# Kernel tuning notes

Hardware: AMD Instinct MI355X
Metric: run time of the kernel (lower is better)

## Reference

```python
import jax, jax.numpy as jnp
import numpy as np

NUM = 5   # grid intervals
K = 3     # spline order


def make_grid(in_dim, num=NUM, k=K, lo=-1.0, hi=1.0):
    # pykan: linspace over [lo,hi] with num+1 knots, extended by k on each side
    g = np.linspace(lo, hi, num + 1)
    h = (g[-1] - g[0]) / num
    left = g[0] - h * np.arange(k, 0, -1)
    right = g[-1] + h * np.arange(1, k + 1)
    g = np.concatenate([left, g, right])  # (num + 2k + 1,)
    return jnp.asarray(np.broadcast_to(g, (in_dim, g.shape[0])), dtype=jnp.float32)


def b_batch(x, grid, k=K):
    # x: (B, in), grid: (in, G) -> B-spline bases (B, in, G-k-1) via Cox-de Boor
    xe = x[:, :, None]                      # (B, in, 1)
    g = grid[None]                          # (1, in, G)
    B = ((xe >= g[:, :, :-1]) & (xe < g[:, :, 1:])).astype(x.dtype)
    for ki in range(1, k + 1):
        B = ((xe - g[:, :, :-(ki + 1)]) / (g[:, :, ki:-1] - g[:, :, :-(ki + 1)]) * B[:, :, :-1]
             + (g[:, :, ki + 1:] - xe) / (g[:, :, ki + 1:] - g[:, :, 1:-ki]) * B[:, :, 1:])
    return jnp.nan_to_num(B)


def kan_layer(x, grid, coef, scale_base, scale_sp, mask, k=K):
    # x: (B, in); coef: (in, out, num+k); scales/mask: (in, out)
    base = jax.nn.silu(x)                             # (B, in)
    Bsp = b_batch(x, grid, k)                         # (B, in, num+k)
    y = jnp.einsum('bik,iok->bio', Bsp, coef)         # spline curves (B, in, out)
    y = scale_base[None] * base[:, :, None] + scale_sp[None] * y
    y = mask[None] * y
    return jnp.sum(y, axis=1)                         # (B, out)


def setup_inputs() -> dict:
    key = jax.random.key(0)
    ks = jax.random.split(key, 10)
    B, IN, HID, OUT = 4096, 1024, 256, 128
    KC = NUM + K  # coef count per edge
    x = jax.random.normal(ks[0], (B, IN), dtype=jnp.float32)
    W1 = jax.random.normal(ks[1], (HID, IN), dtype=jnp.float32) / np.sqrt(IN)
    b1 = jnp.zeros((HID,), dtype=jnp.float32)
    grid1 = make_grid(HID)
    coef1 = jax.random.normal(ks[2], (HID, HID, KC), dtype=jnp.float32) * 0.1
    sb1 = jax.random.normal(ks[3], (HID, HID), dtype=jnp.float32) / np.sqrt(HID)
    sp1 = jnp.ones((HID, HID), dtype=jnp.float32) / np.sqrt(HID)
    mask1 = jnp.ones((HID, HID), dtype=jnp.float32)
    grid2 = make_grid(HID)
    coef2 = jax.random.normal(ks[4], (HID, OUT, KC), dtype=jnp.float32) * 0.1
    sb2 = jax.random.normal(ks[5], (HID, OUT), dtype=jnp.float32) / np.sqrt(HID)
    sp2 = jnp.ones((HID, OUT), dtype=jnp.float32) / np.sqrt(HID)
    mask2 = jnp.ones((HID, OUT), dtype=jnp.float32)
    return {"x": x, "W1": W1, "b1": b1,
            "grid1": grid1, "coef1": coef1, "sb1": sb1, "sp1": sp1, "mask1": mask1,
            "grid2": grid2, "coef2": coef2, "sb2": sb2, "sp2": sp2, "mask2": mask2}


def reference(x, W1, b1, grid1, coef1, sb1, sp1, mask1, grid2, coef2, sb2, sp2, mask2):
    h = x @ W1.T + b1                                  # fc1
    h = kan_layer(h, grid1, coef1, sb1, sp1, mask1)    # kanl1
    out = kan_layer(h, grid2, coef2, sb2, sp2, mask2)  # kanl2
    return out
```

## Files before the change

### kernel.cpp

```cpp
#include <hip/hip_runtime.h>
#include <math.h>

typedef unsigned short u16;
typedef u16 u16x4 __attribute__((ext_vector_type(4)));
typedef u16 u16x8 __attribute__((ext_vector_type(8)));
typedef float f32x4 __attribute__((ext_vector_type(4)));
typedef float f32x16 __attribute__((ext_vector_type(16)));
typedef __bf16 bf16x8 __attribute__((ext_vector_type(8)));

#define KC 8
#define K2L 2304

__device__ __forceinline__ u16 f2bf_rne(float f) {
  unsigned u = __float_as_uint(f);
  u += 0x7FFFu + ((u >> 16) & 1u);
  return (u16)(u >> 16);
}
__device__ __forceinline__ float bf2f(u16 h) {
  return __uint_as_float(((unsigned)h) << 16);
}

__device__ __forceinline__ void gload16(const u16* g, u16* l) {
  __builtin_amdgcn_global_load_lds(
      (const __attribute__((address_space(1))) unsigned*)g,
      (__attribute__((address_space(3))) unsigned*)l, 16, 0, 0);
}

template <int N>
__device__ __forceinline__ void vmwait() {
  if constexpr (N == 0)      asm volatile("s_waitcnt vmcnt(0)" ::: "memory");
  else if constexpr (N == 4) asm volatile("s_waitcnt vmcnt(4)" ::: "memory");
  else if constexpr (N == 8) asm volatile("s_waitcnt vmcnt(8)" ::: "memory");
  else static_assert(N == 0, "unsupported vmcnt literal");
}

__device__ __forceinline__ void split4(const float* X, u16* hi, u16* lo, int i) {
  f32x4 v = ((const f32x4*)X)[i];
  u16x4 h, l;
#pragma unroll
  for (int c = 0; c < 4; ++c) {
    u16 hb = f2bf_rne(v[c]);
    h[c] = hb;
    l[c] = f2bf_rne(v[c] - bf2f(hb));
  }
  ((u16x4*)hi)[i] = h;
  ((u16x4*)lo)[i] = l;
}
__device__ __forceinline__ void wc_one(const float* coef, const float* sb, const float* sp,
                                       const float* mask, u16* W, int N, int idx) {
  int o = idx / K2L;
  int r = idx - o * K2L;
  int i = r / 9;
  int c = r - i * 9;
  int io = i * N + o;
  float m = mask[io];
  float v = (c == 0) ? m * sb[io] : m * sp[io] * coef[(size_t)io * KC + (c - 1)];
  W[idx] = f2bf_rne(v);
}

__global__ void prep_kernel(const float* __restrict__ x, const float* __restrict__ W1,
                            const float* __restrict__ coef1, const float* __restrict__ sb1,
                            const float* __restrict__ sp1, const float* __restrict__ mask1,
                            const float* __restrict__ coef2, const float* __restrict__ sb2,
                            const float* __restrict__ sp2, const float* __restrict__ mask2,
                            u16* __restrict__ xs_hi, u16* __restrict__ xs_lo,
                            u16* __restrict__ w1_hi, u16* __restrict__ w1_lo,
                            u16* __restrict__ wc1, u16* __restrict__ wc2) {
  const int b = blockIdx.x, tid = threadIdx.x;
  if (b < 4096) {
    split4(x, xs_hi, xs_lo, b * 256 + tid);
  } else if (b < 4096 + 256) {
    split4(W1, w1_hi, w1_lo, (b - 4096) * 256 + tid);
  } else if (b < 4096 + 256 + 2304) {
    wc_one(coef1, sb1, sp1, mask1, wc1, 256, (b - 4352) * 256 + tid);
  } else {
    wc_one(coef2, sb2, sp2, mask2, wc2, 128, (b - 6656) * 256 + tid);
  }
}

struct Spl {
  float g[12];
  float d1[11], d2[10], d3[9];
};
__device__ __forceinline__ void spl_init(const float* __restrict__ grid, Spl& sp) {
#pragma unroll
  for (int j = 0; j < 12; ++j) sp.g[j] = grid[j];
#pragma unroll
  for (int j = 0; j < 11; ++j) sp.d1[j] = 1.0f / (sp.g[j + 1] - sp.g[j]);
#pragma unroll
  for (int j = 0; j < 10; ++j) sp.d2[j] = 1.0f / (sp.g[j + 2] - sp.g[j]);
#pragma unroll
  for (int j = 0; j < 9; ++j) sp.d3[j] = 1.0f / (sp.g[j + 3] - sp.g[j]);
}
__device__ __forceinline__ void expand_one(float v, const Spl& sp, u16* dst) {
  float Bv[11];
#pragma unroll
  for (int j = 0; j < 11; ++j) Bv[j] = (v >= sp.g[j] && v < sp.g[j + 1]) ? 1.0f : 0.0f;
#pragma unroll
  for (int j = 0; j < 10; ++j)
    Bv[j] = (v - sp.g[j]) * sp.d1[j] * Bv[j] + (sp.g[j + 2] - v) * sp.d1[j + 1] * Bv[j + 1];
#pragma unroll
  for (int j = 0; j < 9; ++j)
    Bv[j] = (v - sp.g[j]) * sp.d2[j] * Bv[j] + (sp.g[j + 3] - v) * sp.d2[j + 1] * Bv[j + 1];
#pragma unroll
  for (int j = 0; j < 8; ++j)
    Bv[j] = (v - sp.g[j]) * sp.d3[j] * Bv[j] + (sp.g[j + 4] - v) * sp.d3[j + 1] * Bv[j + 1];
  dst[0] = f2bf_rne(v / (1.0f + __expf(-v)));
#pragma unroll
  for (int k = 0; k < 8; ++k) dst[1 + k] = f2bf_rne(Bv[k]);
}

template <int NREG, bool EXPAND>
__global__ __launch_bounds__(512) void gemm8w(
    const u16* __restrict__ A0, const u16* __restrict__ A1,
    const u16* __restrict__ B0, const u16* __restrict__ B1,
    const float* __restrict__ bias, const float* __restrict__ grid,
    void* __restrict__ outv, int M, int N, int K, int nsteps) {
  constexpr int ASZ = 64 * 128;
  constexpr int BUF_U16 = 2 * ASZ;
  __shared__ __align__(16) u16 smu[4 * BUF_U16];

  const int tid = threadIdx.x;
  const int lane = tid & 63;
  const int wid = tid >> 6;
  const int q = wid & 3;
  const int kg = wid >> 2;

  const int nb = N >> 6;
  const int nwg = (M >> 6) * nb;
  const int bid = blockIdx.x;
  const int swz = (bid & 7) * (nwg >> 3) + (bid >> 3);
  const int tm = (swz / nb) << 6;
  const int tn = (swz % nb) << 6;

  const u16* pA0 = A0 + (size_t)tm * K;
  const u16* pB0 = B0 + (size_t)tn * K;
  const u16* pA1 = (NREG == 3) ? A1 + (size_t)tm * K : nullptr;
  const u16* pB1 = (NREG == 3) ? B1 + (size_t)tn * K : nullptr;

  auto srcOff = [&](int c) -> int {
    int r = c >> 4, sl = c & 15;
    return r * K + (((sl ^ (r & 15)) & 15) << 3);
  };
  const int s0 = srcOff(tid);
  const int s1 = srcOff(tid + 512);

  const int wm = (q >> 1) * 32;
  const int wn = (q & 1) * 32;
  const int lr = lane & 31;
  const int khf = lane >> 5;

  int offA[4], offB[4];
#pragma unroll
  for (int s = 0; s < 4; ++s) {
    int slice = kg * 4 + s;
    int rowA = wm + lr;
    int rowB = wn + lr;
    offA[s] = rowA * 128 + ((((slice * 2 + khf) ^ (rowA & 15)) & 15) << 3);
    offB[s] = rowB * 128 + ((((slice * 2 + khf) ^ (rowB & 15)) & 15) << 3);
  }

  auto stage = [&](int buf, int step) {
    int kk;
    const u16 *Ab, *Bb;
    if constexpr (NREG == 3) {
      int reg = step >> 3;
      kk = (step & 7) << 7;
      Ab = (reg == 2) ? pA1 : pA0;
      Bb = (reg == 1) ? pB1 : pB0;
    } else {
      kk = step << 7;
      Ab = pA0;
      Bb = pB0;
    }
    u16* sb = smu + buf * BUF_U16;
    gload16(Ab + s0 + kk, sb + wid * 512);
    gload16(Ab + s1 + kk, sb + 4096 + wid * 512);
    gload16(Bb + s0 + kk, sb + ASZ + wid * 512);
    gload16(Bb + s1 + kk, sb + ASZ + 4096 + wid * 512);
  };

  f32x16 acc0 = {}, acc1 = {};
  stage(0, 0);
  stage(1, 1);
  for (int i = 0; i < nsteps; ++i) {
    if (i + 2 < nsteps) {
      stage((i + 2) & 3, i + 2);
      vmwait<8>();
    } else if (i + 1 < nsteps) {
      vmwait<4>();
    } else {
      vmwait<0>();
    }
    __builtin_amdgcn_sched_barrier(0);
    __builtin_amdgcn_s_barrier();
    __builtin_amdgcn_sched_barrier(0);

    const u16* sb = smu + (i & 3) * BUF_U16;
    bf16x8 af[4], bfr[4];
#pragma unroll
    for (int s = 0; s < 4; ++s) {
      af[s] = *(const bf16x8*)(sb + offA[s]);
      bfr[s] = *(const bf16x8*)(sb + ASZ + offB[s]);
    }
#pragma unroll
    for (int s = 0; s < 4; ++s) {
      f32x16& ac = (s & 1) ? acc1 : acc0;
      ac = __builtin_amdgcn_mfma_f32_32x32x16_bf16(af[s], bfr[s], ac, 0, 0, 0);
    }
  }
  f32x16 accv = acc0 + acc1;

  const int rbase = 4 * khf;

  float* Fr = (float*)smu;
  __syncthreads();
  if (kg == 1) {
#pragma unroll
    for (int r = 0; r < 16; ++r) {
      int row = wm + rbase + (r & 3) + 8 * (r >> 2);
      Fr[row * 64 + wn + lr] = accv[r];
    }
  }
  __syncthreads();
  if (kg == 0) {
#pragma unroll
    for (int r = 0; r < 16; ++r) {
      int row = wm + rbase + (r & 3) + 8 * (r >> 2);
      accv[r] += Fr[row * 64 + wn + lr];
    }
  }

  if constexpr (EXPAND) {
    Spl sp;
    spl_init(grid, sp);
    __syncthreads();
    u16* Fl = smu;
    if (kg == 0) {
      int col = wn + lr;
      float bv = bias ? bias[tn + col] : 0.0f;
#pragma unroll
      for (int r = 0; r < 16; ++r) {
        int row = wm + rbase + (r & 3) + 8 * (r >> 2);
        expand_one(accv[r] + bv, sp, Fl + (size_t)row * (64 * 9) + col * 9);
      }
    }
    __syncthreads();
    u16* Fout = (u16*)outv;
    const size_t fstride = (size_t)N * 9;
#pragma unroll
    for (int ch = tid; ch < 4608; ch += 512) {
      int r = ch / 72, o = ch - r * 72;
      *(u16x8*)(Fout + (size_t)(tm + r) * fstride + (size_t)tn * 9 + o * 8) =
          *(const u16x8*)(Fl + (size_t)ch * 8);
    }
  } else {
    if (kg == 0) {
      float* Cp = (float*)outv;
      const int cbase = tn + wn + lr;
#pragma unroll
      for (int r = 0; r < 16; ++r) {
        int row = tm + wm + rbase + (r & 3) + 8 * (r >> 2);
        Cp[(size_t)row * N + cbase] = accv[r];
      }
    }
  }
}

extern "C" void kernel_launch(void* const* d_in, const int* in_sizes, int n_in,
                              void* d_out, int out_size, void* d_ws, size_t ws_size,
                              hipStream_t stream) {
  (void)in_sizes; (void)n_in; (void)out_size; (void)ws_size;
  const float* x     = (const float*)d_in[0];
  const float* W1    = (const float*)d_in[1];
  const float* b1    = (const float*)d_in[2];
  const float* grid1 = (const float*)d_in[3];
  const float* coef1 = (const float*)d_in[4];
  const float* sb1   = (const float*)d_in[5];
  const float* sp1   = (const float*)d_in[6];
  const float* mask1 = (const float*)d_in[7];
  const float* grid2 = (const float*)d_in[8];
  const float* coef2 = (const float*)d_in[9];
  const float* sb2   = (const float*)d_in[10];
  const float* sp2   = (const float*)d_in[11];
  const float* mask2 = (const float*)d_in[12];
  float* outp = (float*)d_out;

  char* ws = (char*)d_ws;
  size_t off = 0;
  auto alloc = [&](size_t bytes) {
    char* p = ws + off;
    off += (bytes + 255) & ~(size_t)255;
    return (void*)p;
  };
  u16* xs_hi  = (u16*)alloc((size_t)4096 * 1024 * 2);
  u16* xs_lo  = (u16*)alloc((size_t)4096 * 1024 * 2);
  u16* w1_hi  = (u16*)alloc((size_t)256 * 1024 * 2);
  u16* w1_lo  = (u16*)alloc((size_t)256 * 1024 * 2);
  u16* wc1    = (u16*)alloc((size_t)256 * K2L * 2);
  u16* wc2    = (u16*)alloc((size_t)128 * K2L * 2);
  u16* F1     = (u16*)alloc((size_t)4096 * K2L * 2);
  u16* F2     = (u16*)alloc((size_t)4096 * K2L * 2);

  prep_kernel<<<7808, 256, 0, stream>>>(x, W1, coef1, sb1, sp1, mask1,
                                        coef2, sb2, sp2, mask2,
                                        xs_hi, xs_lo, w1_hi, w1_lo, wc1, wc2);

  gemm8w<3, true><<<256, 512, 0, stream>>>(
      xs_hi, xs_lo, w1_hi, w1_lo, b1, grid1, F1, 4096, 256, 1024, 24);

  gemm8w<1, true><<<256, 512, 0, stream>>>(
      F1, nullptr, wc1, nullptr, nullptr, grid2, F2, 4096, 256, 2304, 18);

  gemm8w<1, false><<<128, 512, 0, stream>>>(
      F2, nullptr, wc2, nullptr, nullptr, nullptr, outp, 4096, 128, 2304, 18);
}
```

Baseline: 68.81 us.

## Use 16-wave workgroups with 256-wide K steps and double buffering

The three GEMM kernels go from 8 waves (512 threads) to 16 waves (1024 threads) per workgroup, and each step now stages a 256-wide K slice instead of a 128-wide one. The loop count halves, and the K split spans four wave groups, which adds an extra shared-memory reduction stage at the end. The pipeline moves from a 4-buffer, two-ahead prefetch to a 2-buffer scheme that waits for vmcnt(0) at every step before issuing the next load. The aim is more waves per CU to hide latency and fewer barriers, but prefetch depth is lower and exposed load latency may rise.

New measurement: 73.12 us. 1.06x slower.

```diff
diff --git a/kernel.cpp b/kernel.cpp
--- a/kernel.cpp
+++ b/kernel.cpp
@@ -25,13 +25,8 @@
       (const __attribute__((address_space(1))) unsigned*)g,
       (__attribute__((address_space(3))) unsigned*)l, 16, 0, 0);
 }
-
-template <int N>
-__device__ __forceinline__ void vmwait() {
-  if constexpr (N == 0)      asm volatile("s_waitcnt vmcnt(0)" ::: "memory");
-  else if constexpr (N == 4) asm volatile("s_waitcnt vmcnt(4)" ::: "memory");
-  else if constexpr (N == 8) asm volatile("s_waitcnt vmcnt(8)" ::: "memory");
-  else static_assert(N == 0, "unsupported vmcnt literal");
+__device__ __forceinline__ void vmwait0() {
+  asm volatile("s_waitcnt vmcnt(0)" ::: "memory");
 }
 
 __device__ __forceinline__ void split4(const float* X, u16* hi, u16* lo, int i) {
@@ -111,14 +106,14 @@
 }
 
 template <int NREG, bool EXPAND>
-__global__ __launch_bounds__(512) void gemm8w(
+__global__ __launch_bounds__(1024) void gemm16w(
     const u16* __restrict__ A0, const u16* __restrict__ A1,
     const u16* __restrict__ B0, const u16* __restrict__ B1,
     const float* __restrict__ bias, const float* __restrict__ grid,
     void* __restrict__ outv, int M, int N, int K, int nsteps) {
-  constexpr int ASZ = 64 * 128;
+  constexpr int ASZ = 64 * 256;
   constexpr int BUF_U16 = 2 * ASZ;
-  __shared__ __align__(16) u16 smu[4 * BUF_U16];
+  __shared__ __align__(16) u16 smu[2 * BUF_U16];
 
   const int tid = threadIdx.x;
   const int lane = tid & 63;
@@ -139,11 +134,11 @@
   const u16* pB1 = (NREG == 3) ? B1 + (size_t)tn * K : nullptr;
 
   auto srcOff = [&](int c) -> int {
-    int r = c >> 4, sl = c & 15;
-    return r * K + (((sl ^ (r & 15)) & 15) << 3);
+    int r = c >> 5, sl = c & 31;
+    return r * K + (((sl ^ (r & 31)) & 31) << 3);
   };
   const int s0 = srcOff(tid);
-  const int s1 = srcOff(tid + 512);
+  const int s1 = srcOff(tid + 1024);
 
   const int wm = (q >> 1) * 32;
   const int wn = (q & 1) * 32;
@@ -156,47 +151,40 @@
     int slice = kg * 4 + s;
     int rowA = wm + lr;
     int rowB = wn + lr;
-    offA[s] = rowA * 128 + ((((slice * 2 + khf) ^ (rowA & 15)) & 15) << 3);
-    offB[s] = rowB * 128 + ((((slice * 2 + khf) ^ (rowB & 15)) & 15) << 3);
+    offA[s] = rowA * 256 + ((((slice * 2 + khf) ^ (rowA & 31)) & 31) << 3);
+    offB[s] = rowB * 256 + ((((slice * 2 + khf) ^ (rowB & 31)) & 31) << 3);
   }
 
   auto stage = [&](int buf, int step) {
     int kk;
     const u16 *Ab, *Bb;
     if constexpr (NREG == 3) {
-      int reg = step >> 3;
-      kk = (step & 7) << 7;
+      int reg = step >> 2;
+      kk = (step & 3) << 8;
       Ab = (reg == 2) ? pA1 : pA0;
       Bb = (reg == 1) ? pB1 : pB0;
     } else {
-      kk = step << 7;
+      kk = step << 8;
       Ab = pA0;
       Bb = pB0;
     }
     u16* sb = smu + buf * BUF_U16;
     gload16(Ab + s0 + kk, sb + wid * 512);
-    gload16(Ab + s1 + kk, sb + 4096 + wid * 512);
+    gload16(Ab + s1 + kk, sb + 8192 + wid * 512);
     gload16(Bb + s0 + kk, sb + ASZ + wid * 512);
-    gload16(Bb + s1 + kk, sb + ASZ + 4096 + wid * 512);
+    gload16(Bb + s1 + kk, sb + ASZ + 8192 + wid * 512);
   };
 
   f32x16 acc0 = {}, acc1 = {};
   stage(0, 0);
-  stage(1, 1);
   for (int i = 0; i < nsteps; ++i) {
-    if (i + 2 < nsteps) {
-      stage((i + 2) & 3, i + 2);
-      vmwait<8>();
-    } else if (i + 1 < nsteps) {
-      vmwait<4>();
-    } else {
-      vmwait<0>();
-    }
+    vmwait0();
     __builtin_amdgcn_sched_barrier(0);
     __builtin_amdgcn_s_barrier();
     __builtin_amdgcn_sched_barrier(0);
-
-    const u16* sb = smu + (i & 3) * BUF_U16;
+    if (i + 1 < nsteps) stage((i + 1) & 1, i + 1);
+
+    const u16* sb = smu + (i & 1) * BUF_U16;
     bf16x8 af[4], bfr[4];
 #pragma unroll
     for (int s = 0; s < 4; ++s) {
@@ -214,6 +202,22 @@
   const int rbase = 4 * khf;
 
   float* Fr = (float*)smu;
+  __syncthreads();
+  if (kg >= 2) {
+#pragma unroll
+    for (int r = 0; r < 16; ++r) {
+      int row = wm + rbase + (r & 3) + 8 * (r >> 2);
+      Fr[(kg - 2) * 4096 + row * 64 + wn + lr] = accv[r];
+    }
+  }
+  __syncthreads();
+  if (kg < 2) {
+#pragma unroll
+    for (int r = 0; r < 16; ++r) {
+      int row = wm + rbase + (r & 3) + 8 * (r >> 2);
+      accv[r] += Fr[kg * 4096 + row * 64 + wn + lr];
+    }
+  }
   __syncthreads();
   if (kg == 1) {
 #pragma unroll
@@ -249,7 +253,7 @@
     u16* Fout = (u16*)outv;
     const size_t fstride = (size_t)N * 9;
 #pragma unroll
-    for (int ch = tid; ch < 4608; ch += 512) {
+    for (int ch = tid; ch < 4608; ch += 1024) {
       int r = ch / 72, o = ch - r * 72;
       *(u16x8*)(Fout + (size_t)(tm + r) * fstride + (size_t)tn * 9 + o * 8) =
           *(const u16x8*)(Fl + (size_t)ch * 8);
@@ -306,12 +310,12 @@
                                         coef2, sb2, sp2, mask2,
                                         xs_hi, xs_lo, w1_hi, w1_lo, wc1, wc2);
 
-  gemm8w<3, true><<<256, 512, 0, stream>>>(
-      xs_hi, xs_lo, w1_hi, w1_lo, b1, grid1, F1, 4096, 256, 1024, 24);
-
-  gemm8w<1, true><<<256, 512, 0, stream>>>(
-      F1, nullptr, wc1, nullptr, nullptr, grid2, F2, 4096, 256, 2304, 18);
-
-  gemm8w<1, false><<<128, 512, 0, stream>>>(
-      F2, nullptr, wc2, nullptr, nullptr, nullptr, outp, 4096, 128, 2304, 18);
-}
+  gemm16w<3, true><<<256, 1024, 0, stream>>>(
+      xs_hi, xs_lo, w1_hi, w1_lo, b1, grid1, F1, 4096, 256, 1024, 12);
+
+  gemm16w<1, true><<<256, 1024, 0, stream>>>(
+      F1, nullptr, wc1, nullptr, nullptr, grid2, F2, 4096, 256, 2304, 9);
+
+  gemm16w<1, false><<<128, 1024, 0, stream>>>(
+      F2, nullptr, wc2, nullptr, nullptr, nullptr, outp, 4096, 128, 2304, 9);
+}
```

## Shrink GEMM tiles to 64x32/32x64 with 4-way K split and triple buffering

Applied to the files above, without the earlier changes.

Replaces the 64x64 output tile GEMM with a templated kernel using 64x32 (or 32x64) tiles, doubling the workgroup count so more CUs are occupied on the small M=4096 problems. Each wave now handles two K-slices per step instead of four, giving a 4-way intra-block K split that needs an extra LDS reduction round. The LDS pipeline changes from 4 buffers to 3, with prefetch issued after the barrier. The trade-off is less data reuse per tile, more redundant operand loads and extra reduction synchronisation.

After: 76.10 us. 1.11x slower.

```diff
diff --git a/kernel.cpp b/kernel.cpp
--- a/kernel.cpp
+++ b/kernel.cpp
@@ -25,12 +25,10 @@
       (const __attribute__((address_space(1))) unsigned*)g,
       (__attribute__((address_space(3))) unsigned*)l, 16, 0, 0);
 }
-
 template <int N>
 __device__ __forceinline__ void vmwait() {
   if constexpr (N == 0)      asm volatile("s_waitcnt vmcnt(0)" ::: "memory");
-  else if constexpr (N == 4) asm volatile("s_waitcnt vmcnt(4)" ::: "memory");
-  else if constexpr (N == 8) asm volatile("s_waitcnt vmcnt(8)" ::: "memory");
+  else if constexpr (N == 3) asm volatile("s_waitcnt vmcnt(3)" ::: "memory");
   else static_assert(N == 0, "unsupported vmcnt literal");
 }
 
@@ -110,52 +108,57 @@
   for (int k = 0; k < 8; ++k) dst[1 + k] = f2bf_rne(Bv[k]);
 }
 
-template <int NREG, bool EXPAND>
-__global__ __launch_bounds__(512) void gemm8w(
+template <int NREG, int MQ, int NQ, bool EXPAND>
+__global__ __launch_bounds__(512) void gemmS(
     const u16* __restrict__ A0, const u16* __restrict__ A1,
     const u16* __restrict__ B0, const u16* __restrict__ B1,
     const float* __restrict__ bias, const float* __restrict__ grid,
     void* __restrict__ outv, int M, int N, int K, int nsteps) {
-  constexpr int ASZ = 64 * 128;
-  constexpr int BUF_U16 = 2 * ASZ;
-  __shared__ __align__(16) u16 smu[4 * BUF_U16];
+  constexpr int BM = MQ * 32, BN = NQ * 32;
+  constexpr int ASZ = BM * 128;
+  constexpr int BUF_U16 = (BM + BN) * 128;
+  __shared__ __align__(16) u16 smu[3 * BUF_U16];
 
   const int tid = threadIdx.x;
   const int lane = tid & 63;
   const int wid = tid >> 6;
-  const int q = wid & 3;
-  const int kg = wid >> 2;
-
-  const int nb = N >> 6;
-  const int nwg = (M >> 6) * nb;
+  const int mq = (MQ == 2) ? (wid & 1) : 0;
+  const int nq = (NQ == 2) ? (wid & 1) : 0;
+  const int kg = wid >> 1;
+
+  const int nb = N / BN;
+  const int nwg = (M / BM) * nb;
   const int bid = blockIdx.x;
   const int swz = (bid & 7) * (nwg >> 3) + (bid >> 3);
-  const int tm = (swz / nb) << 6;
-  const int tn = (swz % nb) << 6;
+  const int tm = (swz / nb) * BM;
+  const int tn = (swz % nb) * BN;
 
   const u16* pA0 = A0 + (size_t)tm * K;
   const u16* pB0 = B0 + (size_t)tn * K;
   const u16* pA1 = (NREG == 3) ? A1 + (size_t)tm * K : nullptr;
   const u16* pB1 = (NREG == 3) ? B1 + (size_t)tn * K : nullptr;
 
-  auto srcOff = [&](int c) -> int {
-    int r = c >> 4, sl = c & 15;
-    return r * K + (((sl ^ (r & 15)) & 15) << 3);
-  };
-  const int s0 = srcOff(tid);
-  const int s1 = srcOff(tid + 512);
-
-  const int wm = (q >> 1) * 32;
-  const int wn = (q & 1) * 32;
+  int srcO[3];
+  bool isA[3];
+#pragma unroll
+  for (int k = 0; k < 3; ++k) {
+    int c = tid + k * 512;
+    bool a = c < BM * 16;
+    int r = a ? (c >> 4) : ((c - BM * 16) >> 4);
+    int sl = c & 15;
+    isA[k] = a;
+    srcO[k] = r * K + (((sl ^ (r & 15)) & 15) << 3);
+  }
+
   const int lr = lane & 31;
   const int khf = lane >> 5;
 
-  int offA[4], offB[4];
-#pragma unroll
-  for (int s = 0; s < 4; ++s) {
-    int slice = kg * 4 + s;
-    int rowA = wm + lr;
-    int rowB = wn + lr;
+  int offA[2], offB[2];
+#pragma unroll
+  for (int s = 0; s < 2; ++s) {
+    int slice = kg * 2 + s;
+    int rowA = mq * 32 + lr;
+    int rowB = nq * 32 + lr;
     offA[s] = rowA * 128 + ((((slice * 2 + khf) ^ (rowA & 15)) & 15) << 3);
     offB[s] = rowB * 128 + ((((slice * 2 + khf) ^ (rowB & 15)) & 15) << 3);
   }
@@ -174,60 +177,72 @@
       Bb = pB0;
     }
     u16* sb = smu + buf * BUF_U16;
-    gload16(Ab + s0 + kk, sb + wid * 512);
-    gload16(Ab + s1 + kk, sb + 4096 + wid * 512);
-    gload16(Bb + s0 + kk, sb + ASZ + wid * 512);
-    gload16(Bb + s1 + kk, sb + ASZ + 4096 + wid * 512);
+#pragma unroll
+    for (int k = 0; k < 3; ++k)
+      gload16((isA[k] ? Ab : Bb) + srcO[k] + kk, sb + (k * 512 + wid * 64) * 8);
   };
 
   f32x16 acc0 = {}, acc1 = {};
   stage(0, 0);
   stage(1, 1);
+  int cur = 0, b3 = 2;
   for (int i = 0; i < nsteps; ++i) {
-    if (i + 2 < nsteps) {
-      stage((i + 2) & 3, i + 2);
-      vmwait<8>();
-    } else if (i + 1 < nsteps) {
-      vmwait<4>();
-    } else {
-      vmwait<0>();
-    }
+    if (i + 1 < nsteps) vmwait<3>();
+    else vmwait<0>();
     __builtin_amdgcn_sched_barrier(0);
     __builtin_amdgcn_s_barrier();
     __builtin_amdgcn_sched_barrier(0);
-
-    const u16* sb = smu + (i & 3) * BUF_U16;
-    bf16x8 af[4], bfr[4];
-#pragma unroll
-    for (int s = 0; s < 4; ++s) {
+    if (i + 2 < nsteps) stage(b3, i + 2);
+
+    const u16* sb = smu + cur * BUF_U16;
+    bf16x8 af[2], bfr[2];
+#pragma unroll
+    for (int s = 0; s < 2; ++s) {
       af[s] = *(const bf16x8*)(sb + offA[s]);
       bfr[s] = *(const bf16x8*)(sb + ASZ + offB[s]);
     }
-#pragma unroll
-    for (int s = 0; s < 4; ++s) {
-      f32x16& ac = (s & 1) ? acc1 : acc0;
-      ac = __builtin_amdgcn_mfma_f32_32x32x16_bf16(af[s], bfr[s], ac, 0, 0, 0);
-    }
+    acc0 = __builtin_amdgcn_mfma_f32_32x32x16_bf16(af[0], bfr[0], acc0, 0, 0, 0);
+    acc1 = __builtin_amdgcn_mfma_f32_32x32x16_bf16(af[1], bfr[1], acc1, 0, 0, 0);
+
+    cur = (cur == 2) ? 0 : cur + 1;
+    b3 = (b3 == 2) ? 0 : b3 + 1;
   }
   f32x16 accv = acc0 + acc1;
 
   const int rbase = 4 * khf;
+  const int rowq = mq * 32, colq = nq * 32;
 
   float* Fr = (float*)smu;
   __syncthreads();
+  if (kg >= 2) {
+#pragma unroll
+    for (int r = 0; r < 16; ++r) {
+      int row = rowq + rbase + (r & 3) + 8 * (r >> 2);
+      Fr[(kg - 2) * (BM * BN) + row * BN + colq + lr] = accv[r];
+    }
+  }
+  __syncthreads();
+  if (kg < 2) {
+#pragma unroll
+    for (int r = 0; r < 16; ++r) {
+      int row = rowq + rbase + (r & 3) + 8 * (r >> 2);
+      accv[r] += Fr[kg * (BM * BN) + row * BN + colq + lr];
+    }
+  }
+  __syncthreads();
   if (kg == 1) {
 #pragma unroll
     for (int r = 0; r < 16; ++r) {
-      int row = wm + rbase + (r & 3) + 8 * (r >> 2);
-      Fr[row * 64 + wn + lr] = accv[r];
+      int row = rowq + rbase + (r & 3) + 8 * (r >> 2);
+      Fr[row * BN + colq + lr] = accv[r];
     }
   }
   __syncthreads();
   if (kg == 0) {
 #pragma unroll
     for (int r = 0; r < 16; ++r) {
-      int row = wm + rbase + (r & 3) + 8 * (r >> 2);
-      accv[r] += Fr[row * 64 + wn + lr];
+      int row = rowq + rbase + (r & 3) + 8 * (r >> 2);
+      accv[r] += Fr[row * BN + colq + lr];
     }
   }
 
@@ -237,30 +252,31 @@
     __syncthreads();
     u16* Fl = smu;
     if (kg == 0) {
-      int col = wn + lr;
+      int col = colq + lr;
       float bv = bias ? bias[tn + col] : 0.0f;
 #pragma unroll
       for (int r = 0; r < 16; ++r) {
-        int row = wm + rbase + (r & 3) + 8 * (r >> 2);
-        expand_one(accv[r] + bv, sp, Fl + (size_t)row * (64 * 9) + col * 9);
+        int row = rowq + rbase + (r & 3) + 8 * (r >> 2);
+        expand_one(accv[r] + bv, sp, Fl + (size_t)row * (BN * 9) + col * 9);
       }
     }
     __syncthreads();
     u16* Fout = (u16*)outv;
+    constexpr int RB = BN * 9 / 8;
+    constexpr int CH = BM * RB;
     const size_t fstride = (size_t)N * 9;
-#pragma unroll
-    for (int ch = tid; ch < 4608; ch += 512) {
-      int r = ch / 72, o = ch - r * 72;
+    for (int ch = tid; ch < CH; ch += 512) {
+      int r = ch / RB, o = ch - r * RB;
       *(u16x8*)(Fout + (size_t)(tm + r) * fstride + (size_t)tn * 9 + o * 8) =
           *(const u16x8*)(Fl + (size_t)ch * 8);
     }
   } else {
     if (kg == 0) {
       float* Cp = (float*)outv;
-      const int cbase = tn + wn + lr;
+      const int cbase = tn + colq + lr;
 #pragma unroll
       for (int r = 0; r < 16; ++r) {
-        int row = tm + wm + rbase + (r & 3) + 8 * (r >> 2);
+        int row = tm + rowq + rbase + (r & 3) + 8 * (r >> 2);
         Cp[(size_t)row * N + cbase] = accv[r];
       }
     }
@@ -306,12 +322,12 @@
                                         coef2, sb2, sp2, mask2,
                                         xs_hi, xs_lo, w1_hi, w1_lo, wc1, wc2);
 
-  gemm8w<3, true><<<256, 512, 0, stream>>>(
+  gemmS<3, 2, 1, true><<<512, 512, 0, stream>>>(
       xs_hi, xs_lo, w1_hi, w1_lo, b1, grid1, F1, 4096, 256, 1024, 24);
 
-  gemm8w<1, true><<<256, 512, 0, stream>>>(
+  gemmS<1, 2, 1, true><<<512, 512, 0, stream>>>(
       F1, nullptr, wc1, nullptr, nullptr, grid2, F2, 4096, 256, 2304, 18);
 
-  gemm8w<1, false><<<128, 512, 0, stream>>>(
+  gemmS<1, 1, 2, false><<<256, 512, 0, stream>>>(
       F2, nullptr, wc2, nullptr, nullptr, nullptr, outp, 4096, 128, 2304, 18);
 }
```
